# Kernel tuning notes

Hardware: AMD Instinct MI355X
Metric: run time of the kernel (lower is better)

Reference implementation:

```python
import jax, jax.numpy as jnp
import numpy as np

E, B, D, T = 8, 4096, 2048, 2048
H = D // 2 + T // 2  # expert hidden dim = 2048
TOP_K = 2


def setup_inputs() -> dict:
    key = jax.random.key(0)
    ks = jax.random.split(key, 5)
    s_in = 1.0 / np.sqrt(D)
    s_h = 1.0 / np.sqrt(H)
    return {
        "xs": jax.random.normal(ks[0], (E, B, D), dtype=jnp.float32),
        "Wg": jax.random.normal(ks[1], (D,), dtype=jnp.float32) * s_in,
        "bg": jnp.zeros((1,), dtype=jnp.float32),
        "W1": jax.random.normal(ks[2], (E, D, H), dtype=jnp.float32) * s_in,
        "b1": jnp.zeros((E, H), dtype=jnp.float32),
        "W2": jax.random.normal(ks[3], (E, H, T), dtype=jnp.float32) * s_h,
        "b2": jnp.zeros((E, T), dtype=jnp.float32),
    }


def reference(xs, Wg, bg, W1, b1, W2, b2):
    # Gating: logits[b, e] = x[e][b] @ Wg + bg  -> [B, E]
    logits = jnp.einsum("ebd,d->be", xs, Wg) + bg
    probs = jax.nn.softmax(logits, axis=1)
    top_k_values, top_k_indices = jax.lax.top_k(probs, TOP_K)  # [B, K]

    # Dense expert compute over each expert's own input stream.
    # hidden[e, b, h] = relu(x[e] @ W1[e] + b1[e]); out[e, b, t] = hidden @ W2[e] + b2[e]
    hidden = jax.nn.relu(jnp.einsum("ebd,edh->ebh", xs, W1) + b1[:, None, :])
    expert_out = jnp.einsum("ebh,eht->ebt", hidden, W2) + b2[:, None, :]  # [E, B, T]

    # Gather the top-k experts per token. In the original, masked-dense compute
    # + output mask is mathematically identical to this gather.
    per_token = jnp.transpose(expert_out, (1, 0, 2))  # [B, E, T]
    selected = jnp.take_along_axis(per_token, top_k_indices[:, :, None], axis=1)  # [B, K, T]

    out = jnp.sum(top_k_values[:, :, None] * selected, axis=1)  # [B, T]
    return out, top_k_values
```

## Files before the change

kernel.cpp:

```cpp
#include <hip/hip_runtime.h>
#include <hip/hip_bf16.h>
#include <stdint.h>

#define E_ 8
#define B_ 4096
#define D_ 2048
#define T_ 2048
#define H_ 2048
#define KDIM 2048
#define NDIM 2048
#define ECAP 2048
#define GEMM_BLKS (39 * 8)

typedef __attribute__((ext_vector_type(4))) float f32x4;
typedef __attribute__((ext_vector_type(4))) unsigned short u16x4;
typedef __attribute__((ext_vector_type(8))) unsigned short u16x8;
typedef __attribute__((ext_vector_type(8))) __bf16 bf16x8;

__device__ __forceinline__ unsigned short f2bf(float f) {
    __hip_bfloat16 h = __float2bfloat16(f);
    return __builtin_bit_cast(unsigned short, h);
}

__device__ __forceinline__ void gload_lds16(const void* g, void* lds) {
    __builtin_amdgcn_global_load_lds(
        (const __attribute__((address_space(1))) void*)g,
        (__attribute__((address_space(3))) void*)lds, 16, 0, 0);
}

__global__ __launch_bounds__(256) void fused_pre(
    const float* __restrict__ xs, const float* __restrict__ Wg,
    const float* __restrict__ bg,
    const float* __restrict__ W1,
    unsigned short* __restrict__ Wt1,
    float* __restrict__ out_topk, int* __restrict__ counts,
    unsigned short* __restrict__ Axf, int* __restrict__ tokf,
    float* __restrict__ probf, int nwt)
{
    const int bid = blockIdx.x;
    const int t = threadIdx.x;

    __shared__ __align__(16) unsigned char smem[33024];

    if (bid < nwt) {
        const int e   = bid >> 10;
        const int rem = bid & 1023;
        const int kb  = ((rem >> 5) & 31) << 6;
        const int nb  = (rem & 31) << 6;

        float (*tile)[65] = (float(*)[65])smem;
        const float* src = W1 + ((size_t)e * KDIM + kb) * NDIM + nb;
        {
            const int kr = t >> 2, nc = (t & 3) * 16;
            #pragma unroll
            for (int j = 0; j < 4; ++j) {
                f32x4 v = __builtin_nontemporal_load(
                    (const f32x4*)(src + (size_t)kr * NDIM + nc + j * 4));
                tile[kr][nc + j*4 + 0] = v.x;
                tile[kr][nc + j*4 + 1] = v.y;
                tile[kr][nc + j*4 + 2] = v.z;
                tile[kr][nc + j*4 + 3] = v.w;
            }
        }
        __syncthreads();
        {
            const int nn = t >> 2, kc = (t & 3) * 16;
            unsigned short wbuf[16];
            #pragma unroll
            for (int j = 0; j < 16; ++j) wbuf[j] = f2bf(tile[kc + j][nn]);
            unsigned short* dst =
                Wt1 + ((size_t)e * NDIM + nb + nn) * KDIM + kb + kc;
            *(u16x8*)dst       = *(const u16x8*)&wbuf[0];
            *((u16x8*)dst + 1) = *(const u16x8*)&wbuf[8];
        }
        return;
    }

    const int b = bid - nwt;
    const int wave = t >> 6, lane = t & 63;
    unsigned short* xrow = (unsigned short*)smem;
    float (*red)[4]      = (float(*)[4])(smem + 32768);
    int* shi             = (int*)(smem + 32768 + 128);

    const f32x4 wg0 = ((const f32x4*)Wg)[t];
    const f32x4 wg1 = ((const f32x4*)Wg)[t + 256];

    #pragma unroll
    for (int e = 0; e < E_; ++e) {
        const f32x4* xr = (const f32x4*)(xs + ((size_t)e * B_ + b) * D_);
        f32x4 a0 = __builtin_nontemporal_load(&xr[t]);
        f32x4 a1 = __builtin_nontemporal_load(&xr[t + 256]);
        float p = a0.x*wg0.x + a0.y*wg0.y + a0.z*wg0.z + a0.w*wg0.w
                + a1.x*wg1.x + a1.y*wg1.y + a1.z*wg1.z + a1.w*wg1.w;
        u16x4 w;
        w[0]=f2bf(a0.x); w[1]=f2bf(a0.y); w[2]=f2bf(a0.z); w[3]=f2bf(a0.w);
        *(u16x4*)(xrow + e * 2048 + 4 * t) = w;
        w[0]=f2bf(a1.x); w[1]=f2bf(a1.y); w[2]=f2bf(a1.z); w[3]=f2bf(a1.w);
        *(u16x4*)(xrow + e * 2048 + 1024 + 4 * t) = w;
        #pragma unroll
        for (int off = 32; off >= 1; off >>= 1) p += __shfl_xor(p, off);
        if (lane == 0) red[e][wave] = p;
    }
    __syncthreads();
    if (t == 0) {
        float pr[E_];
        float mx = -3.0e38f;
        #pragma unroll
        for (int e = 0; e < E_; ++e) {
            pr[e] = red[e][0] + red[e][1] + red[e][2] + red[e][3] + bg[0];
            mx = fmaxf(mx, pr[e]);
        }
        float s = 0.f;
        #pragma unroll
        for (int e = 0; e < E_; ++e) { pr[e] = expf(pr[e] - mx); s += pr[e]; }
        float inv = 1.0f / s;
        #pragma unroll
        for (int e = 0; e < E_; ++e) pr[e] *= inv;
        int i0 = 0;
        #pragma unroll
        for (int e = 1; e < E_; ++e) if (pr[e] > pr[i0]) i0 = e;
        int i1 = (i0 == 0) ? 1 : 0;
        #pragma unroll
        for (int e = 0; e < E_; ++e) { if (e != i0 && pr[e] > pr[i1]) i1 = e; }
        float p0 = pr[i0], p1 = pr[i1];
        out_topk[2*b]   = p0;
        out_topk[2*b+1] = p1;
        int pos0 = atomicAdd(&counts[i0], 1);
        int pos1 = atomicAdd(&counts[i1], 1);
        if (pos0 >= ECAP) pos0 = ECAP - 1;
        if (pos1 >= ECAP) pos1 = ECAP - 1;
        tokf[i0 * ECAP + pos0] = b;  probf[i0 * ECAP + pos0] = p0;
        tokf[i1 * ECAP + pos1] = b;  probf[i1 * ECAP + pos1] = p1;
        shi[0] = i0; shi[1] = i1; shi[2] = pos0; shi[3] = pos1;
    }
    __syncthreads();
    const int i0 = shi[0], i1 = shi[1], p0 = shi[2], p1 = shi[3];

    {
        u16x8 v = *(const u16x8*)(xrow + (size_t)i0 * 2048 + 8 * t);
        ((u16x8*)(Axf + (size_t)(i0 * ECAP + p0) * D_))[t] = v;
    }
    {
        u16x8 v = *(const u16x8*)(xrow + (size_t)i1 * 2048 + 8 * t);
        ((u16x8*)(Axf + (size_t)(i1 * ECAP + p1) * D_))[t] = v;
    }
}

__global__ __launch_bounds__(256) void wtrans1(
    const float* __restrict__ W, unsigned short* __restrict__ Wt)
{
    const int e  = blockIdx.z;
    const int kb = blockIdx.x * 64;
    const int nb = blockIdx.y * 64;
    const int t  = threadIdx.x;
    __shared__ float tile[64][65];

    const float* src = W + ((size_t)e * KDIM + kb) * NDIM + nb;
    {
        const int kr = t >> 2, nc = (t & 3) * 16;
        #pragma unroll
        for (int j = 0; j < 4; ++j) {
            f32x4 v = __builtin_nontemporal_load(
                (const f32x4*)(src + (size_t)kr * NDIM + nc + j * 4));
            tile[kr][nc + j*4 + 0] = v.x;
            tile[kr][nc + j*4 + 1] = v.y;
            tile[kr][nc + j*4 + 2] = v.z;
            tile[kr][nc + j*4 + 3] = v.w;
        }
    }
    __syncthreads();
    {
        const int nn = t >> 2, kc = (t & 3) * 16;
        unsigned short wbuf[16];
        #pragma unroll
        for (int j = 0; j < 16; ++j) wbuf[j] = f2bf(tile[kc + j][nn]);
        unsigned short* dst = Wt + ((size_t)e * NDIM + nb + nn) * KDIM + kb + kc;
        *(u16x8*)dst       = *(const u16x8*)&wbuf[0];
        *((u16x8*)dst + 1) = *(const u16x8*)&wbuf[8];
    }
}

#define BAR  __builtin_amdgcn_s_barrier()

template<int LAYER>
__global__ __launch_bounds__(1024, 4) void moe_gemm(
    const unsigned short* __restrict__ Abuf,
    const unsigned short* __restrict__ Wt,
    const float* __restrict__ bias,
    const int* __restrict__ counts,
    const int* __restrict__ tokf,
    const float* __restrict__ probf,
    unsigned short* __restrict__ hidden_out,
    float* __restrict__ out,
    const float* __restrict__ Wsrc2,
    unsigned short* __restrict__ Wt2dst,
    int gemmBlks)
{
    const int bid = blockIdx.x;
    const int t = threadIdx.x;

    __shared__ u16x8 As[4 * 1024];
    __shared__ u16x8 Bs[4 * 1024];

    if (LAYER == 1 && bid >= gemmBlks) {
        float (*tile)[65] = (float(*)[65])&As[0];
        const int wb = bid - gemmBlks;
        #pragma unroll 1
        for (int i = 0; i < 8; ++i) {
            const int tau = wb * 8 + i;
            const int e2  = tau >> 10;
            const int rem = tau & 1023;
            const int kb  = ((rem >> 5) & 31) << 6;
            const int nb  = (rem & 31) << 6;
            const float* src = Wsrc2 + ((size_t)e2 * KDIM + kb) * NDIM + nb;
            {
                const int kr = t >> 4, nc = (t & 15) * 4;
                f32x4 v = __builtin_nontemporal_load(
                    (const f32x4*)(src + (size_t)kr * NDIM + nc));
                tile[kr][nc+0] = v.x; tile[kr][nc+1] = v.y;
                tile[kr][nc+2] = v.z; tile[kr][nc+3] = v.w;
            }
            __syncthreads();
            {
                const int nn = t >> 4, kc = (t & 15) * 4;
                u16x4 wv;
                wv[0]=f2bf(tile[kc+0][nn]); wv[1]=f2bf(tile[kc+1][nn]);
                wv[2]=f2bf(tile[kc+2][nn]); wv[3]=f2bf(tile[kc+3][nn]);
                *(u16x4*)(Wt2dst + ((size_t)e2 * NDIM + nb + nn) * KDIM + kb + kc) = wv;
            }
            __syncthreads();
        }
        return;
    }

    const int mt  = bid >> 3;
    const int np  = bid & 7;

    int nMt = 0, base = 0;
    int e = -1, mloc = 0, eb = 0, n_e = 0;
    #pragma unroll
    for (int ee = 0; ee < E_; ++ee) {
        int ce = counts[ee]; if (ce > ECAP) ce = ECAP;
        int te = (ce + 255) >> 8;
        if (e < 0 && mt < nMt + te) {
            e = ee; mloc = (mt - nMt) * 256; eb = base; n_e = ce;
        }
        nMt += te;
        base += ce;
    }
    if (mt >= nMt) return;

    const int arow0 = (LAYER == 1) ? (e * ECAP + mloc) : (eb + mloc);
    const int n0 = np * 256;

    const int lane = t & 63;
    const int w = t >> 6;
    const int wm = (w >> 2) * 64;
    const int wn = (w & 3) * 64;
    const int lg = lane >> 4;

    const int ksw = (((t & 3) ^ ((t >> 3) & 3)) << 3);
    const unsigned short* aptr = Abuf + (size_t)(arow0 + (t >> 2)) * KDIM + ksw;
    const unsigned short* bptr =
        Wt + ((size_t)e * NDIM + n0 + (t >> 2)) * KDIM + ksw;

#define STG(BUF, KT) do{ \
    gload_lds16(aptr + (KT)*32, &As[(BUF)*1024 + w*64]); \
    gload_lds16(bptr + (KT)*32, &Bs[(BUF)*1024 + w*64]); }while(0)

    f32x4 acc[4][4];
    #pragma unroll
    for (int i = 0; i < 4; ++i)
        #pragma unroll
        for (int j = 0; j < 4; ++j) {
            f32x4 z = {0.f, 0.f, 0.f, 0.f};
            acc[i][j] = z;
        }

    STG(0, 0); STG(1, 1); STG(2, 2);

    const int usw = (lane >> 1) & 3;
    for (int kt = 0; kt < 64; ++kt) {
        asm volatile("s_waitcnt vmcnt(4)" ::: "memory");
        BAR;
        int tn = kt + 3; if (tn > 63) tn = 63;
        STG((kt + 3) & 3, tn);

        const int bse = (kt & 3) * 1024;
        bf16x8 af[4];
        #pragma unroll
        for (int mi = 0; mi < 4; ++mi) {
            const int row = wm + mi * 16 + (lane & 15);
            af[mi] = __builtin_bit_cast(bf16x8, As[bse + row * 4 + (lg ^ usw)]);
        }
        #pragma unroll
        for (int ni = 0; ni < 4; ++ni) {
            const int row = wn + ni * 16 + (lane & 15);
            bf16x8 bq = __builtin_bit_cast(bf16x8, Bs[bse + row * 4 + (lg ^ usw)]);
            #pragma unroll
            for (int mi = 0; mi < 4; ++mi)
                acc[mi][ni] = __builtin_amdgcn_mfma_f32_16x16x32_bf16(
                    af[mi], bq, acc[mi][ni], 0, 0, 0);
        }
    }
    asm volatile("s_waitcnt vmcnt(0)" ::: "memory");

    #pragma unroll
    for (int mi = 0; mi < 4; ++mi) {
        #pragma unroll
        for (int rr = 0; rr < 4; ++rr) {
            const int rloc = wm + mi * 16 + ((lane >> 4) << 2) + rr;
            if (mloc + rloc >= n_e) continue;
            #pragma unroll
            for (int ni = 0; ni < 4; ++ni) {
                const int col = n0 + wn + ni * 16 + (lane & 15);
                float v = acc[mi][ni][rr];
                if (LAYER == 1) {
                    v += bias[e * NDIM + col];
                    v = fmaxf(v, 0.f);
                    hidden_out[(size_t)(eb + mloc + rloc) * H_ + col] = f2bf(v);
                } else {
                    const int f = e * ECAP + mloc + rloc;
                    v = (v + bias[e * NDIM + col]) * probf[f];
                    atomicAdd(&out[(size_t)tokf[f] * T_ + col], v);
                }
            }
        }
    }
#undef STG
}

extern "C" void kernel_launch(void* const* d_in, const int* in_sizes, int n_in,
                              void* d_out, int out_size, void* d_ws, size_t ws_size,
                              hipStream_t stream)
{
    const float* xs = (const float*)d_in[0];
    const float* Wg = (const float*)d_in[1];
    const float* bg = (const float*)d_in[2];
    const float* W1 = (const float*)d_in[3];
    const float* b1 = (const float*)d_in[4];
    const float* W2 = (const float*)d_in[5];
    const float* b2 = (const float*)d_in[6];

    float* out      = (float*)d_out;
    float* out_topk = out + (size_t)B_ * T_;

    char* ws = (char*)d_ws;
    int*   counts = (int*)ws;
    int*   tokf   = (int*)(ws + 1024);
    float* probf  = (float*)(ws + 1024 + E_ * ECAP * 4);
    size_t off = 1024 + (size_t)E_ * ECAP * 8;
    off = (off + 255) & ~(size_t)255;
    unsigned short* Axf    = (unsigned short*)(ws + off); off += (size_t)E_ * ECAP * D_ * 2;
    unsigned short* hidden = (unsigned short*)(ws + off); off += (size_t)(2 * B_ + 256) * H_ * 2;
    unsigned short* Wt1    = (unsigned short*)(ws + off); off += (size_t)E_ * KDIM * NDIM * 2;
    size_t off_big = off + (size_t)E_ * KDIM * NDIM * 2;
    unsigned short* Wt2 = (unsigned short*)(ws + off);

    const bool big = (ws_size >= off_big);

    hipMemsetAsync(counts, 0, 256, stream);
    hipMemsetAsync(out, 0, (size_t)B_ * T_ * sizeof(float), stream);

    dim3 blk(256), gblk(1024);

    if (big) {
        const int nwt = 8 * 1024;
        fused_pre<<<dim3(nwt + B_), blk, 0, stream>>>(
            xs, Wg, bg, W1, Wt1, out_topk, counts, Axf, tokf, probf, nwt);
        moe_gemm<1><<<dim3(GEMM_BLKS + 1024), gblk, 0, stream>>>(
            Axf, Wt1, b1, counts, tokf, probf, hidden, nullptr,
            W2, Wt2, GEMM_BLKS);
        moe_gemm<2><<<dim3(GEMM_BLKS), gblk, 0, stream>>>(
            hidden, Wt2, b2, counts, tokf, probf, nullptr, out,
            nullptr, nullptr, GEMM_BLKS);
    } else {
        dim3 tgrid(32, 32, E_);
        fused_pre<<<dim3(B_), blk, 0, stream>>>(
            xs, Wg, bg, W1, Wt1, out_topk, counts, Axf, tokf, probf, 0);
        wtrans1<<<tgrid, blk, 0, stream>>>(W1, Wt1);
        moe_gemm<1><<<dim3(GEMM_BLKS), gblk, 0, stream>>>(
            Axf, Wt1, b1, counts, tokf, probf, hidden, nullptr,
            nullptr, nullptr, GEMM_BLKS);
        wtrans1<<<tgrid, blk, 0, stream>>>(W2, Wt1);
        moe_gemm<2><<<dim3(GEMM_BLKS), gblk, 0, stream>>>(
            hidden, Wt1, b2, counts, tokf, probf, nullptr, out,
            nullptr, nullptr, GEMM_BLKS);
    }
}
```

Baseline: 453.0 us.

## Fuse both expert GEMM layers into one persistent-ticket kernel with per-expert flags

Merges the layer-1 GEMM, the W2 transpose/convert, and the layer-2 GEMM into a single launch. Blocks take work in order through an atomic ticket counter. Layer-2 tiles spin-wait on per-expert counters that record finished layer-1 tiles and finished W2 transpose chunks. The goal is to remove the kernel boundary and the tail bubble between the layers, letting layer-2 work for early experts overlap with the rest of layer 1. In exchange it adds atomics, fences and spin-waits, and ticket ordering is needed to avoid deadlock. LAYER is now a runtime value, which may affect code generation.

```diff
diff --git a/kernel.cpp b/kernel.cpp
--- a/kernel.cpp
+++ b/kernel.cpp
@@ -11,6 +11,7 @@
 #define NDIM 2048
 #define ECAP 2048
 #define GEMM_BLKS (39 * 8)
+#define WT_BLKS 1024
 
 typedef __attribute__((ext_vector_type(4))) float f32x4;
 typedef __attribute__((ext_vector_type(4))) unsigned short u16x4;
@@ -135,7 +136,6 @@
     }
     __syncthreads();
     const int i0 = shi[0], i1 = shi[1], p0 = shi[2], p1 = shi[3];
-
     {
         u16x8 v = *(const u16x8*)(xrow + (size_t)i0 * 2048 + 8 * t);
         ((u16x8*)(Axf + (size_t)(i0 * ECAP + p0) * D_))[t] = v;
@@ -182,29 +182,34 @@
 
 #define BAR  __builtin_amdgcn_s_barrier()
 
-template<int LAYER>
-__global__ __launch_bounds__(1024, 4) void moe_gemm(
-    const unsigned short* __restrict__ Abuf,
-    const unsigned short* __restrict__ Wt,
-    const float* __restrict__ bias,
+__global__ __launch_bounds__(1024, 4) void moe_fused(
+    const unsigned short* __restrict__ Axf,
+    const unsigned short* __restrict__ hidden_r,
+    unsigned short* __restrict__ hidden_w,
+    const unsigned short* __restrict__ Wt1,
+    unsigned short* __restrict__ Wt2,
+    const float* __restrict__ b1, const float* __restrict__ b2,
     const int* __restrict__ counts,
     const int* __restrict__ tokf,
     const float* __restrict__ probf,
-    unsigned short* __restrict__ hidden_out,
     float* __restrict__ out,
-    const float* __restrict__ Wsrc2,
-    unsigned short* __restrict__ Wt2dst,
-    int gemmBlks)
+    const float* __restrict__ W2src,
+    int* __restrict__ ticket, int* __restrict__ done1, int* __restrict__ wdone,
+    int g1Blks, int wtBlks, int doWait)
 {
-    const int bid = blockIdx.x;
     const int t = threadIdx.x;
-
     __shared__ u16x8 As[4 * 1024];
     __shared__ u16x8 Bs[4 * 1024];
-
-    if (LAYER == 1 && bid >= gemmBlks) {
+    __shared__ int sh_tk;
+
+    if (t == 0) sh_tk = atomicAdd(ticket, 1);
+    __syncthreads();
+    const int tk = sh_tk;
+
+    if (tk >= g1Blks && tk < g1Blks + wtBlks) {
         float (*tile)[65] = (float(*)[65])&As[0];
-        const int wb = bid - gemmBlks;
+        const int wb = tk - g1Blks;
+        int e2last = -1;
         #pragma unroll 1
         for (int i = 0; i < 8; ++i) {
             const int tau = wb * 8 + i;
@@ -212,7 +217,8 @@
             const int rem = tau & 1023;
             const int kb  = ((rem >> 5) & 31) << 6;
             const int nb  = (rem & 31) << 6;
-            const float* src = Wsrc2 + ((size_t)e2 * KDIM + kb) * NDIM + nb;
+            e2last = e2;
+            const float* src = W2src + ((size_t)e2 * KDIM + kb) * NDIM + nb;
             {
                 const int kr = t >> 4, nc = (t & 15) * 4;
                 f32x4 v = __builtin_nontemporal_load(
@@ -226,15 +232,22 @@
                 u16x4 wv;
                 wv[0]=f2bf(tile[kc+0][nn]); wv[1]=f2bf(tile[kc+1][nn]);
                 wv[2]=f2bf(tile[kc+2][nn]); wv[3]=f2bf(tile[kc+3][nn]);
-                *(u16x4*)(Wt2dst + ((size_t)e2 * NDIM + nb + nn) * KDIM + kb + kc) = wv;
+                *(u16x4*)(Wt2 + ((size_t)e2 * NDIM + nb + nn) * KDIM + kb + kc) = wv;
             }
             __syncthreads();
         }
+        __threadfence();
+        __syncthreads();
+        if (t == 0)
+            __hip_atomic_fetch_add(&wdone[e2last], 1,
+                __ATOMIC_RELEASE, __HIP_MEMORY_SCOPE_AGENT);
         return;
     }
 
-    const int mt  = bid >> 3;
-    const int np  = bid & 7;
+    const int LAYER = (tk < g1Blks) ? 1 : 2;
+    const int gb = (LAYER == 1) ? tk : (tk - g1Blks - wtBlks);
+    const int mt = gb >> 3;
+    const int np = gb & 7;
 
     int nMt = 0, base = 0;
     int e = -1, mloc = 0, eb = 0, n_e = 0;
@@ -250,6 +263,22 @@
     }
     if (mt >= nMt) return;
 
+    if (LAYER == 2 && doWait) {
+        const int need1 = ((n_e + 255) >> 8) * 8;
+        if (t == 0) {
+            while (__hip_atomic_load(&done1[e],
+                    __ATOMIC_ACQUIRE, __HIP_MEMORY_SCOPE_AGENT) < need1)
+                __builtin_amdgcn_s_sleep(8);
+            while (__hip_atomic_load(&wdone[e],
+                    __ATOMIC_ACQUIRE, __HIP_MEMORY_SCOPE_AGENT) < 128)
+                __builtin_amdgcn_s_sleep(8);
+        }
+        __syncthreads();
+    }
+
+    const unsigned short* Abuf = (LAYER == 1) ? Axf : hidden_r;
+    const unsigned short* Wt   = (LAYER == 1) ? Wt1 : Wt2;
+    const float* bias          = (LAYER == 1) ? b1  : b2;
     const int arow0 = (LAYER == 1) ? (e * ECAP + mloc) : (eb + mloc);
     const int n0 = np * 256;
 
@@ -318,7 +347,7 @@
                 if (LAYER == 1) {
                     v += bias[e * NDIM + col];
                     v = fmaxf(v, 0.f);
-                    hidden_out[(size_t)(eb + mloc + rloc) * H_ + col] = f2bf(v);
+                    hidden_w[(size_t)(eb + mloc + rloc) * H_ + col] = f2bf(v);
                 } else {
                     const int f = e * ECAP + mloc + rloc;
                     v = (v + bias[e * NDIM + col]) * probf[f];
@@ -326,6 +355,14 @@
                 }
             }
         }
+    }
+
+    if (LAYER == 1 && doWait) {
+        __threadfence();
+        __syncthreads();
+        if (t == 0)
+            __hip_atomic_fetch_add(&done1[e], 1,
+                __ATOMIC_RELEASE, __HIP_MEMORY_SCOPE_AGENT);
     }
 #undef STG
 }
@@ -347,6 +384,9 @@
 
     char* ws = (char*)d_ws;
     int*   counts = (int*)ws;
+    int*   done1  = (int*)(ws + 256);
+    int*   wdone  = (int*)(ws + 288);
+    int*   tickets= (int*)(ws + 320);
     int*   tokf   = (int*)(ws + 1024);
     float* probf  = (float*)(ws + 1024 + E_ * ECAP * 4);
     size_t off = 1024 + (size_t)E_ * ECAP * 8;
@@ -359,7 +399,7 @@
 
     const bool big = (ws_size >= off_big);
 
-    hipMemsetAsync(counts, 0, 256, stream);
+    hipMemsetAsync(ws, 0, 1024, stream);
     hipMemsetAsync(out, 0, (size_t)B_ * T_ * sizeof(float), stream);
 
     dim3 blk(256), gblk(1024);
@@ -368,23 +408,20 @@
         const int nwt = 8 * 1024;
         fused_pre<<<dim3(nwt + B_), blk, 0, stream>>>(
             xs, Wg, bg, W1, Wt1, out_topk, counts, Axf, tokf, probf, nwt);
-        moe_gemm<1><<<dim3(GEMM_BLKS + 1024), gblk, 0, stream>>>(
-            Axf, Wt1, b1, counts, tokf, probf, hidden, nullptr,
-            W2, Wt2, GEMM_BLKS);
-        moe_gemm<2><<<dim3(GEMM_BLKS), gblk, 0, stream>>>(
-            hidden, Wt2, b2, counts, tokf, probf, nullptr, out,
-            nullptr, nullptr, GEMM_BLKS);
+        moe_fused<<<dim3(GEMM_BLKS + WT_BLKS + GEMM_BLKS), gblk, 0, stream>>>(
+            Axf, hidden, hidden, Wt1, Wt2, b1, b2, counts, tokf, probf, out,
+            W2, &tickets[0], done1, wdone, GEMM_BLKS, WT_BLKS, 1);
     } else {
         dim3 tgrid(32, 32, E_);
         fused_pre<<<dim3(B_), blk, 0, stream>>>(
             xs, Wg, bg, W1, Wt1, out_topk, counts, Axf, tokf, probf, 0);
         wtrans1<<<tgrid, blk, 0, stream>>>(W1, Wt1);
-        moe_gemm<1><<<dim3(GEMM_BLKS), gblk, 0, stream>>>(
-            Axf, Wt1, b1, counts, tokf, probf, hidden, nullptr,
-            nullptr, nullptr, GEMM_BLKS);
+        moe_fused<<<dim3(GEMM_BLKS), gblk, 0, stream>>>(
+            Axf, hidden, hidden, Wt1, Wt1, b1, b2, counts, tokf, probf, out,
+            nullptr, &tickets[1], done1, wdone, GEMM_BLKS, 0, 0);
         wtrans1<<<tgrid, blk, 0, stream>>>(W2, Wt1);
-        moe_gemm<2><<<dim3(GEMM_BLKS), gblk, 0, stream>>>(
-            hidden, Wt1, b2, counts, tokf, probf, nullptr, out,
-            nullptr, nullptr, GEMM_BLKS);
-    }
-}
+        moe_fused<<<dim3(GEMM_BLKS), gblk, 0, stream>>>(
+            Axf, hidden, hidden, Wt1, Wt1, b1, b2, counts, tokf, probf, out,
+            nullptr, &tickets[2], done1, wdone, 0, 0, 0);
+    }
+}
```

Measured after the change: 1.097 ms. 142% more time.
